# Kernel tuning notes

Measured on AMD Instinct MI355X. Metric: run time of the kernel, lower is better.

The kernel has to match this reference:

```python
import jax, jax.numpy as jnp
import numpy as np

B, S, D = 8, 2048, 2048
E, R, K = 8, 16, 2
NUM_TASKS, NUM_MODES = 4, 2
ALPHA = 16.0


def setup_inputs() -> dict:
    key = jax.random.key(0)
    k1, k2, k3, k4 = jax.random.split(key, 4)
    hidden_states = jax.random.normal(k1, (B, S, D), dtype=jnp.float32)
    gate_w = jax.random.normal(k2, (E, D), dtype=jnp.float32) * 0.01  # nn.init.normal_(std=0.01)
    # Soft-prior biases: fill(-1.0), strong prior 3.0 / 2.0 at configured (task, expert) / (mode, expert)
    tb = -np.ones((NUM_TASKS, E), dtype=np.float32)
    mb = -np.ones((NUM_MODES, E), dtype=np.float32)
    for e in range(E):
        tb[e % NUM_TASKS, e] = 3.0
        mb[e % NUM_MODES, e] = 2.0
    # LoRA params; lora_B is zero-init in torch but we use small random values for a nontrivial baseline
    lora_A = jax.random.normal(k3, (E, R, D), dtype=jnp.float32) * (1.0 / np.sqrt(D))
    lora_B = jax.random.normal(k4, (E, D, R), dtype=jnp.float32) * 0.02
    return {
        "hidden_states": hidden_states,
        "gate_w": gate_w,
        "task_bias": jnp.asarray(tb),
        "mode_bias": jnp.asarray(mb),
        "lora_A": lora_A,
        "lora_B": lora_B,
        "task_id": 1,
        "mode_id": 1,
    }


def reference(hidden_states, gate_w, task_bias, mode_bias, lora_A, lora_B, task_id, mode_id):
    scaling = ALPHA / R
    # Router: score = dynamic_gate(mean_pool(x)) + task_bias[t] + mode_bias[m]
    x_pooled = hidden_states.mean(axis=1)                       # [B, D]
    logits = x_pooled @ gate_w.T + task_bias[task_id] + mode_bias[mode_id]  # [B, E]
    top_v, top_i = jax.lax.top_k(logits, K)                     # [B, K]
    weights = jax.nn.softmax(top_v, axis=-1)                    # [B, K]
    # per-sample, per-expert combine weight: sum of top-k weights routed to that expert
    one_hot = jax.nn.one_hot(top_i, E, dtype=weights.dtype)     # [B, K, E]
    sw = jnp.einsum('bke,bk->be', one_hot, weights)             # [B, E]
    # LoRA experts: (x @ A_e^T) @ B_e^T * scaling, weighted-summed per sample
    mid = jnp.einsum('bsd,erd->besr', hidden_states, lora_A)    # [B, E, S, R] (small: R=16)
    out = jnp.einsum('be,besr,edr->bsd', sw, mid, lora_B) * scaling  # [B, S, D]
    return out
```

## Files before the change

kernel.cpp:

```cpp
#include <hip/hip_runtime.h>
#include <stdint.h>

typedef __attribute__((ext_vector_type(8))) short bf16x8;
typedef __attribute__((ext_vector_type(4))) float f32x4;
typedef __attribute__((ext_vector_type(16))) float f32x16;
typedef unsigned short ushort_t;

#define B_ 8
#define S_ 2048
#define D_ 2048
#define E_ 8
#define J_ 128
#define M_ 64
#define AROWS 136
#define ATILE (AROWS * 64)

static __device__ __forceinline__ unsigned short f2bf(float f) {
  union { float f; uint32_t u; } v; v.f = f;
  uint32_t u = v.u;
  return (unsigned short)((u + 0x7FFFu + ((u >> 16) & 1u)) >> 16);
}
static __device__ __forceinline__ float bf2f(ushort_t h) {
  union { uint32_t u; float f; } v; v.u = ((uint32_t)h) << 16;
  return v.f;
}
static __device__ __forceinline__ uint32_t pkbf(float a, float b) {
  uint32_t r;
  asm("v_cvt_pk_bf16_f32 %0, %1, %2" : "=v"(r) : "v"(a), "v"(b));
  return r;
}
static __device__ __forceinline__ int xswz(int row) {
  return (row & 7) ^ (((row >> 3) & 3) << 1);
}

#define GLL16(gsrc, ldst)                                                        \
  __builtin_amdgcn_global_load_lds(                                              \
      (const __attribute__((address_space(1))) void*)(gsrc),                     \
      (__attribute__((address_space(3))) void*)(ldst), 16, 0, 0)

#define SBAR() __builtin_amdgcn_sched_barrier(0)
#define VMWAIT(N)                                                                \
  do {                                                                           \
    asm volatile("s_waitcnt vmcnt(" #N ")" ::: "memory");                        \
    __builtin_amdgcn_sched_barrier(0);                                           \
  } while (0)
#define VMBAR(N)                                                                 \
  do {                                                                           \
    asm volatile("s_waitcnt vmcnt(" #N ") lgkmcnt(0)\n\ts_barrier" ::: "memory");\
    __builtin_amdgcn_sched_barrier(0);                                           \
  } while (0)

__global__ void k_prep(const float* __restrict__ lA, const float* __restrict__ lB,
                       const float* __restrict__ gw,
                       ushort_t* __restrict__ AgE, ushort_t* __restrict__ Bg) {
  int gid = blockIdx.x * blockDim.x + threadIdx.x;
  int stride = gridDim.x * blockDim.x;
  for (int o = gid; o < 32 * AROWS * 8; o += stride) {
    int kt = o / (AROWS * 8);
    int rem = o - kt * (AROWS * 8);
    int row = rem >> 3, c = rem & 7;
    int d = kt * 64 + (((c ^ xswz(row)) & 7) << 3);
    const float* src = (row < 128) ? (lA + (size_t)row * D_ + d)
                                   : (gw + (size_t)(row - 128) * D_ + d);
    float4 v0 = *(const float4*)src;
    float4 v1 = *(const float4*)(src + 4);
    bf16x8 outv;
    outv[0] = (short)f2bf(v0.x); outv[1] = (short)f2bf(v0.y);
    outv[2] = (short)f2bf(v0.z); outv[3] = (short)f2bf(v0.w);
    outv[4] = (short)f2bf(v1.x); outv[5] = (short)f2bf(v1.y);
    outv[6] = (short)f2bf(v1.z); outv[7] = (short)f2bf(v1.w);
    *(bf16x8*)&AgE[(size_t)o * 8] = outv;
  }
  for (int o4 = gid; o4 < (D_ * J_) / 4; o4 += stride) {
    int j4 = o4 & 31, dd = o4 >> 5;
    int e = j4 >> 2, r0 = (j4 & 3) * 4;
    float4 v = *(const float4*)(lB + ((size_t)e * D_ + dd) * 16 + r0);
    uint2 pk;
    pk.x = (uint32_t)f2bf(v.x) | ((uint32_t)f2bf(v.y) << 16);
    pk.y = (uint32_t)f2bf(v.z) | ((uint32_t)f2bf(v.w) << 16);
    ((uint2*)Bg)[o4] = pk;
  }
}

__global__ __launch_bounds__(512, 2) void k_mid(const float* __restrict__ x,
    const ushort_t* __restrict__ AgE, ushort_t* __restrict__ midb,
    float* __restrict__ lpart) {
  __shared__ ushort_t Ab[3][ATILE];
  __shared__ ushort_t Xb[2][4096];
  __shared__ float lsc[4][8];
  const int tid = threadIdx.x;
  const int w = tid >> 6, lane = tid & 63;
  const int l31 = lane & 31, hi = lane >> 5;
  const int jp = w & 1, xk = w >> 1;
  const int b = blockIdx.y, s0 = blockIdx.x * M_;
  const int xr = tid >> 3;
  const float* xsrc = x + ((size_t)(b * S_ + s0 + xr)) * D_ + (tid & 7) * 8;
  const int xwoff = xr * 64 + ((((tid & 7) ^ xswz(xr)) & 7) << 3);
  const int Xs = xswz(l31);

  f32x16 acc00 = {}, acc01 = {}, acc10 = {}, acc11 = {}, acc2 = {};

  auto stageA = [&](int buf, int kt) {
    const ushort_t* base = AgE + (size_t)kt * ATILE;
    GLL16(base + (size_t)tid * 8, &Ab[buf][tid * 8]);
    GLL16(base + (size_t)(512 + tid) * 8, &Ab[buf][(512 + tid) * 8]);
    GLL16(base + (size_t)(1024 + lane) * 8, &Ab[buf][(1024 + lane) * 8]);
  };
  auto loadX = [&](float4* r4, int t) {
    const float* p = xsrc + t * 64;
    r4[0] = *(const float4*)(p);
    r4[1] = *(const float4*)(p + 4);
  };
  auto cvtWrite = [&](int buf, const float4* r4) {
    uint4 q;
    q.x = pkbf(r4[0].x, r4[0].y); q.y = pkbf(r4[0].z, r4[0].w);
    q.z = pkbf(r4[1].x, r4[1].y); q.w = pkbf(r4[1].z, r4[1].w);
    *(uint4*)&Xb[buf][xwoff] = q;
  };
  auto computeTile = [&](int t, int ab) {
    const int cc = xk * 2 + hi;
    const int chs = (((cc ^ Xs) & 7) << 3);
    const ushort_t* Xp = &Xb[t & 1][l31 * 64 + chs];
    bf16x8 xf0 = *(const bf16x8*)Xp;
    bf16x8 xf1 = *(const bf16x8*)(Xp + 2048);
    const ushort_t* Ap = &Ab[ab][(jp * 64 + l31) * 64 + chs];
    bf16x8 af0 = *(const bf16x8*)Ap;
    bf16x8 af1 = *(const bf16x8*)(Ap + 2048);
    acc00 = __builtin_amdgcn_mfma_f32_32x32x16_bf16(af0, xf0, acc00, 0, 0, 0);
    acc10 = __builtin_amdgcn_mfma_f32_32x32x16_bf16(af0, xf1, acc10, 0, 0, 0);
    acc01 = __builtin_amdgcn_mfma_f32_32x32x16_bf16(af1, xf0, acc01, 0, 0, 0);
    acc11 = __builtin_amdgcn_mfma_f32_32x32x16_bf16(af1, xf1, acc11, 0, 0, 0);
    if (jp == 0) {
      bf16x8 af2 = *(const bf16x8*)&Ab[ab][(128 + l31) * 64 + chs];
      acc2 = __builtin_amdgcn_mfma_f32_32x32x16_bf16(af2, xf0, acc2, 0, 0, 0);
      acc2 = __builtin_amdgcn_mfma_f32_32x32x16_bf16(af2, xf1, acc2, 0, 0, 0);
    }
  };

  float4 xS0[2], xS1[2];
  loadX(xS0, 0); SBAR();
  stageA(0, 0);  SBAR();
  loadX(xS1, 1); SBAR();
  stageA(1, 1);  SBAR();
  VMWAIT(8);
  cvtWrite(0, xS0);
  VMBAR(5);

#define BODY(T, AB, ABN, XCUR, XNXT)                                             \
  do {                                                                           \
    loadX(XNXT, (T) + 2); SBAR();                                                \
    stageA((ABN), (T) + 2); SBAR();                                              \
    computeTile((T), (AB));                                                      \
    VMWAIT(8);                                                                   \
    cvtWrite(((T) + 1) & 1, XCUR);                                               \
    VMBAR(5);                                                                    \
  } while (0)

#pragma unroll 1
  for (int k6 = 0; k6 < 5; ++k6) {
    const int t0 = 6 * k6;
    BODY(t0 + 0, 0, 2, xS1, xS0);
    BODY(t0 + 1, 1, 0, xS0, xS1);
    BODY(t0 + 2, 2, 1, xS1, xS0);
    BODY(t0 + 3, 0, 2, xS0, xS1);
    BODY(t0 + 4, 1, 0, xS1, xS0);
    BODY(t0 + 5, 2, 1, xS0, xS1);
  }
#undef BODY
  computeTile(30, 0);
  VMWAIT(3);
  cvtWrite(1, xS1);
  VMBAR(0);
  computeTile(31, 1);

  __syncthreads();

  if (jp == 0) {
#pragma unroll
    for (int q = 0; q < 4; ++q) {
      float v = acc2[q];
      v += __shfl_xor(v, 1); v += __shfl_xor(v, 2); v += __shfl_xor(v, 4);
      v += __shfl_xor(v, 8); v += __shfl_xor(v, 16);
      if (l31 == 0) lsc[xk][hi * 4 + q] = v;
    }
  }

  float* const reg0 = (float*)&Ab[0][0];
  float* const reg1 = (float*)&Ab[1][0];
#pragma unroll 1
  for (int r = 1; r <= 3; ++r) {
    __syncthreads();
    if (xk == r) {
      float* p = jp ? reg1 : reg0;
#pragma unroll
      for (int i = 0; i < 16; ++i) {
        p[i * 64 + lane]        = acc00[i];
        p[(16 + i) * 64 + lane] = acc01[i];
        p[(32 + i) * 64 + lane] = acc10[i];
        p[(48 + i) * 64 + lane] = acc11[i];
      }
    }
    __syncthreads();
    if (xk == 0) {
      const float* p = jp ? reg1 : reg0;
#pragma unroll
      for (int i = 0; i < 16; ++i) {
        acc00[i] += p[i * 64 + lane];
        acc01[i] += p[(16 + i) * 64 + lane];
        acc10[i] += p[(32 + i) * 64 + lane];
        acc11[i] += p[(48 + i) * 64 + lane];
      }
    }
  }
  __syncthreads();

  if (xk == 0) {
#pragma unroll
    for (int sp = 0; sp < 2; ++sp) {
      ushort_t* mp = midb + ((size_t)(b * S_ + s0 + sp * 32 + l31)) * J_ + jp * 64 + 4 * hi;
#pragma unroll
      for (int G = 0; G < 4; ++G) {
        uint2 pA, pB;
        if (sp == 0) {
          pA.x = pkbf(acc00[G * 4 + 0], acc00[G * 4 + 1]);
          pA.y = pkbf(acc00[G * 4 + 2], acc00[G * 4 + 3]);
          pB.x = pkbf(acc01[G * 4 + 0], acc01[G * 4 + 1]);
          pB.y = pkbf(acc01[G * 4 + 2], acc01[G * 4 + 3]);
        } else {
          pA.x = pkbf(acc10[G * 4 + 0], acc10[G * 4 + 1]);
          pA.y = pkbf(acc10[G * 4 + 2], acc10[G * 4 + 3]);
          pB.x = pkbf(acc11[G * 4 + 0], acc11[G * 4 + 1]);
          pB.y = pkbf(acc11[G * 4 + 2], acc11[G * 4 + 3]);
        }
        *(uint2*)&mp[G * 8] = pA;
        *(uint2*)&mp[32 + G * 8] = pB;
      }
    }
  }
  if (w == 0 && lane < 8) {
    float s = lsc[0][lane] + lsc[1][lane] + lsc[2][lane] + lsc[3][lane];
    lpart[((size_t)(b * 32 + blockIdx.x)) * 8 + lane] = s;
  }
}

__global__ void k_router(const float* __restrict__ lpart,
                         const float* __restrict__ tb, const float* __restrict__ mb,
                         const int* __restrict__ task_p, const int* __restrict__ mode_p,
                         float* __restrict__ rinfo) {
  __shared__ float lg[64];
  const int t = threadIdx.x;
  const int b = t >> 3, e = t & 7;
  float s = 0.f;
  for (int k = 0; k < 32; ++k) s += lpart[((size_t)(b * 32 + k)) * 8 + e];
  lg[t] = s * (1.f / (float)S_) + tb[task_p[0] * E_ + e] + mb[mode_p[0] * E_ + e];
  __syncthreads();
  if (t < B_) {
    float v[8];
#pragma unroll
    for (int e2 = 0; e2 < 8; ++e2) v[e2] = lg[t * 8 + e2];
    int i1 = 0;
#pragma unroll
    for (int e2 = 1; e2 < 8; ++e2) if (v[e2] > v[i1]) i1 = e2;
    int i2 = (i1 == 0) ? 1 : 0;
#pragma unroll
    for (int e2 = 0; e2 < 8; ++e2) if (e2 != i1 && v[e2] > v[i2]) i2 = e2;
    float ex = __expf(v[i2] - v[i1]);
    float w1 = 1.f / (1.f + ex), w2 = ex * w1;
    float4 r;
    r.x = (float)i1; r.y = (float)i2; r.z = w1; r.w = w2;
    ((float4*)rinfo)[t] = r;
  }
}

__global__ __launch_bounds__(256) void k_comb(const ushort_t* __restrict__ midb,
    const float* __restrict__ rinfo, const ushort_t* __restrict__ Bg,
    float* __restrict__ out) {
  __shared__ ushort_t Bt[128][40];
  const int n = blockIdx.x, m = blockIdx.y, b = blockIdx.z;
  const int tid = threadIdx.x, w = tid >> 6, lane = tid & 63;
  const int lm = lane & 15, g = lane >> 4;

  const float4 ri = ((const float4*)rinfo)[b];
  const int i1 = (int)ri.x, i2 = (int)ri.y;
  const float w1 = ri.z, w2 = ri.w;

#pragma unroll
  for (int c = 0; c < 2; ++c) {
    int ci = c * 256 + tid;
    int d = ci >> 2, sub = ci & 3;
    int e = (sub & 2) ? i2 : i1;
    float sc = (sub & 2) ? w2 : w1;
    bf16x8 bv = *(const bf16x8*)(Bg + ((size_t)(n * 128 + d)) * J_ + e * 16 + (sub & 1) * 8);
    bf16x8 bw;
#pragma unroll
    for (int i = 0; i < 8; ++i) bw[i] = (short)f2bf(bf2f((ushort_t)bv[i]) * sc);
    *(bf16x8*)&Bt[d][sub * 8] = bw;
  }

  const int srow = m * 64 + w * 16 + lm;
  const int jw = (g < 2) ? (i1 * 16 + g * 8) : (i2 * 16 + (g - 2) * 8);
  bf16x8 pf = *(const bf16x8*)&midb[((size_t)(b * S_ + srow)) * J_ + jw];
  __syncthreads();

  f32x4 acc[8] = {};
#pragma unroll
  for (int nn = 0; nn < 8; ++nn) {
    bf16x8 af = *(const bf16x8*)&Bt[nn * 16 + lm][g * 8];
    acc[nn] = __builtin_amdgcn_mfma_f32_16x16x32_bf16(af, pf, acc[nn], 0, 0, 0);
  }

  float* op = out + ((size_t)(b * S_ + srow)) * D_ + n * 128;
#pragma unroll
  for (int nn = 0; nn < 8; ++nn)
    *(f32x4*)&op[nn * 16 + g * 4] = acc[nn];
}

extern "C" void kernel_launch(void* const* d_in, const int* in_sizes, int n_in,
                              void* d_out, int out_size, void* d_ws, size_t ws_size,
                              hipStream_t stream) {
  const float* x    = (const float*)d_in[0];
  const float* gw   = (const float*)d_in[1];
  const float* tb   = (const float*)d_in[2];
  const float* mb   = (const float*)d_in[3];
  const float* lA   = (const float*)d_in[4];
  const float* lB   = (const float*)d_in[5];
  const int* task_p = (const int*)d_in[6];
  const int* mode_p = (const int*)d_in[7];
  float* out = (float*)d_out;
  char* ws = (char*)d_ws;
  ushort_t* midb = (ushort_t*)ws;
  ushort_t* AgE  = (ushort_t*)(ws + 4194304);
  ushort_t* Bg   = (ushort_t*)(ws + 4751360);
  float* lpart   = (float*)(ws + 5275648);
  float* rinfo   = (float*)(ws + 5283840);

  hipLaunchKernelGGL(k_prep, dim3(256), dim3(256), 0, stream, lA, lB, gw, AgE, Bg);
  hipLaunchKernelGGL(k_mid, dim3(32, 8), dim3(512), 0, stream, x, AgE, midb, lpart);
  hipLaunchKernelGGL(k_router, dim3(1), dim3(64), 0, stream,
                     lpart, tb, mb, task_p, mode_p, rinfo);
  hipLaunchKernelGGL(k_comb, dim3(16, 32, 8), dim3(256), 0, stream, midb, rinfo, Bg, out);
}
```

Measured before the change: 76.57 us.

## Split k_mid reduction over D across two blocks and sum halves in combine

k_mid now launches a third grid dimension that splits the D reduction into two halves, doubling the block count from 256 to 512 so more CUs get work. Each block writes a partial bf16 mid buffer, and k_comb sums the two halves before its MFMA. Warps are remapped so each owns one 32-row slice and a K-subset, which cuts the in-block cross-warp reduction from three rounds to one. Launch bounds are raised to 4 blocks per CU. The cost is twice the mid write/read traffic, an extra bf16 rounding of the partials, and higher register pressure.

Result: slower. 79.71 us (+4.1%).

```diff
diff --git a/kernel.cpp b/kernel.cpp
--- a/kernel.cpp
+++ b/kernel.cpp
@@ -14,6 +14,7 @@
 #define M_ 64
 #define AROWS 136
 #define ATILE (AROWS * 64)
+#define MIDSZ ((size_t)B_ * S_ * J_)
 
 static __device__ __forceinline__ unsigned short f2bf(float f) {
   union { float f; uint32_t u; } v; v.f = f;
@@ -82,7 +83,7 @@
   }
 }
 
-__global__ __launch_bounds__(512, 2) void k_mid(const float* __restrict__ x,
+__global__ __launch_bounds__(512, 4) void k_mid(const float* __restrict__ x,
     const ushort_t* __restrict__ AgE, ushort_t* __restrict__ midb,
     float* __restrict__ lpart) {
   __shared__ ushort_t Ab[3][ATILE];
@@ -91,17 +92,19 @@
   const int tid = threadIdx.x;
   const int w = tid >> 6, lane = tid & 63;
   const int l31 = lane & 31, hi = lane >> 5;
-  const int jp = w & 1, xk = w >> 1;
+  const int jp = w & 1, sp = (w >> 1) & 1, kk = w >> 2;
   const int b = blockIdx.y, s0 = blockIdx.x * M_;
+  const int kh = blockIdx.z;
   const int xr = tid >> 3;
-  const float* xsrc = x + ((size_t)(b * S_ + s0 + xr)) * D_ + (tid & 7) * 8;
+  const float* xsrc = x + ((size_t)(b * S_ + s0 + xr)) * D_ + kh * 1024 + (tid & 7) * 8;
   const int xwoff = xr * 64 + ((((tid & 7) ^ xswz(xr)) & 7) << 3);
   const int Xs = xswz(l31);
-
-  f32x16 acc00 = {}, acc01 = {}, acc10 = {}, acc11 = {}, acc2 = {};
-
-  auto stageA = [&](int buf, int kt) {
-    const ushort_t* base = AgE + (size_t)kt * ATILE;
+  const ushort_t* Abase = AgE + (size_t)kh * 16 * ATILE;
+
+  f32x16 acc00 = {}, acc01 = {}, acc2 = {};
+
+  auto stageA = [&](int buf, int t) {
+    const ushort_t* base = Abase + (size_t)t * ATILE;
     GLL16(base + (size_t)tid * 8, &Ab[buf][tid * 8]);
     GLL16(base + (size_t)(512 + tid) * 8, &Ab[buf][(512 + tid) * 8]);
     GLL16(base + (size_t)(1024 + lane) * 8, &Ab[buf][(1024 + lane) * 8]);
@@ -118,22 +121,22 @@
     *(uint4*)&Xb[buf][xwoff] = q;
   };
   auto computeTile = [&](int t, int ab) {
-    const int cc = xk * 2 + hi;
-    const int chs = (((cc ^ Xs) & 7) << 3);
-    const ushort_t* Xp = &Xb[t & 1][l31 * 64 + chs];
-    bf16x8 xf0 = *(const bf16x8*)Xp;
-    bf16x8 xf1 = *(const bf16x8*)(Xp + 2048);
-    const ushort_t* Ap = &Ab[ab][(jp * 64 + l31) * 64 + chs];
-    bf16x8 af0 = *(const bf16x8*)Ap;
-    bf16x8 af1 = *(const bf16x8*)(Ap + 2048);
-    acc00 = __builtin_amdgcn_mfma_f32_32x32x16_bf16(af0, xf0, acc00, 0, 0, 0);
-    acc10 = __builtin_amdgcn_mfma_f32_32x32x16_bf16(af0, xf1, acc10, 0, 0, 0);
-    acc01 = __builtin_amdgcn_mfma_f32_32x32x16_bf16(af1, xf0, acc01, 0, 0, 0);
-    acc11 = __builtin_amdgcn_mfma_f32_32x32x16_bf16(af1, xf1, acc11, 0, 0, 0);
-    if (jp == 0) {
-      bf16x8 af2 = *(const bf16x8*)&Ab[ab][(128 + l31) * 64 + chs];
-      acc2 = __builtin_amdgcn_mfma_f32_32x32x16_bf16(af2, xf0, acc2, 0, 0, 0);
-      acc2 = __builtin_amdgcn_mfma_f32_32x32x16_bf16(af2, xf1, acc2, 0, 0, 0);
+    const int xbuf = t & 1;
+#pragma unroll
+    for (int k2 = 0; k2 < 2; ++k2) {
+      const int ks = kk * 2 + k2;
+      const int cc = ks * 2 + hi;
+      const int chs = (((cc ^ Xs) & 7) << 3);
+      bf16x8 xf = *(const bf16x8*)&Xb[xbuf][(sp * 32 + l31) * 64 + chs];
+      const ushort_t* Ap = &Ab[ab][(jp * 64 + l31) * 64 + chs];
+      bf16x8 af0 = *(const bf16x8*)Ap;
+      bf16x8 af1 = *(const bf16x8*)(Ap + 2048);
+      acc00 = __builtin_amdgcn_mfma_f32_32x32x16_bf16(af0, xf, acc00, 0, 0, 0);
+      acc01 = __builtin_amdgcn_mfma_f32_32x32x16_bf16(af1, xf, acc01, 0, 0, 0);
+      if (jp == 0) {
+        bf16x8 af2 = *(const bf16x8*)&Ab[ab][(128 + l31) * 64 + chs];
+        acc2 = __builtin_amdgcn_mfma_f32_32x32x16_bf16(af2, xf, acc2, 0, 0, 0);
+      }
     }
   };
 
@@ -156,22 +159,24 @@
     VMBAR(5);                                                                    \
   } while (0)
 
+  BODY(0, 0, 2, xS1, xS0);
 #pragma unroll 1
-  for (int k6 = 0; k6 < 5; ++k6) {
+  for (int k6 = 0; k6 < 2; ++k6) {
     const int t0 = 6 * k6;
-    BODY(t0 + 0, 0, 2, xS1, xS0);
     BODY(t0 + 1, 1, 0, xS0, xS1);
     BODY(t0 + 2, 2, 1, xS1, xS0);
     BODY(t0 + 3, 0, 2, xS0, xS1);
     BODY(t0 + 4, 1, 0, xS1, xS0);
     BODY(t0 + 5, 2, 1, xS0, xS1);
-  }
+    BODY(t0 + 6, 0, 2, xS1, xS0);
+  }
+  BODY(13, 1, 0, xS0, xS1);
 #undef BODY
-  computeTile(30, 0);
+  computeTile(14, 2);
   VMWAIT(3);
   cvtWrite(1, xS1);
   VMBAR(0);
-  computeTile(31, 1);
+  computeTile(15, 0);
 
   __syncthreads();
 
@@ -181,65 +186,42 @@
       float v = acc2[q];
       v += __shfl_xor(v, 1); v += __shfl_xor(v, 2); v += __shfl_xor(v, 4);
       v += __shfl_xor(v, 8); v += __shfl_xor(v, 16);
-      if (l31 == 0) lsc[xk][hi * 4 + q] = v;
-    }
-  }
-
-  float* const reg0 = (float*)&Ab[0][0];
-  float* const reg1 = (float*)&Ab[1][0];
-#pragma unroll 1
-  for (int r = 1; r <= 3; ++r) {
-    __syncthreads();
-    if (xk == r) {
-      float* p = jp ? reg1 : reg0;
-#pragma unroll
-      for (int i = 0; i < 16; ++i) {
-        p[i * 64 + lane]        = acc00[i];
-        p[(16 + i) * 64 + lane] = acc01[i];
-        p[(32 + i) * 64 + lane] = acc10[i];
-        p[(48 + i) * 64 + lane] = acc11[i];
-      }
-    }
-    __syncthreads();
-    if (xk == 0) {
-      const float* p = jp ? reg1 : reg0;
-#pragma unroll
-      for (int i = 0; i < 16; ++i) {
-        acc00[i] += p[i * 64 + lane];
-        acc01[i] += p[(16 + i) * 64 + lane];
-        acc10[i] += p[(32 + i) * 64 + lane];
-        acc11[i] += p[(48 + i) * 64 + lane];
-      }
+      if (l31 == 0) lsc[sp + 2 * kk][hi * 4 + q] = v;
+    }
+  }
+  float* const scr = (float*)&Ab[0][0];
+  if (kk == 1) {
+    float* p = scr + ((size_t)(w & 3)) * 2048;
+#pragma unroll
+    for (int i = 0; i < 16; ++i) {
+      p[i * 64 + lane]        = acc00[i];
+      p[(16 + i) * 64 + lane] = acc01[i];
     }
   }
   __syncthreads();
-
-  if (xk == 0) {
-#pragma unroll
-    for (int sp = 0; sp < 2; ++sp) {
-      ushort_t* mp = midb + ((size_t)(b * S_ + s0 + sp * 32 + l31)) * J_ + jp * 64 + 4 * hi;
-#pragma unroll
-      for (int G = 0; G < 4; ++G) {
-        uint2 pA, pB;
-        if (sp == 0) {
-          pA.x = pkbf(acc00[G * 4 + 0], acc00[G * 4 + 1]);
-          pA.y = pkbf(acc00[G * 4 + 2], acc00[G * 4 + 3]);
-          pB.x = pkbf(acc01[G * 4 + 0], acc01[G * 4 + 1]);
-          pB.y = pkbf(acc01[G * 4 + 2], acc01[G * 4 + 3]);
-        } else {
-          pA.x = pkbf(acc10[G * 4 + 0], acc10[G * 4 + 1]);
-          pA.y = pkbf(acc10[G * 4 + 2], acc10[G * 4 + 3]);
-          pB.x = pkbf(acc11[G * 4 + 0], acc11[G * 4 + 1]);
-          pB.y = pkbf(acc11[G * 4 + 2], acc11[G * 4 + 3]);
-        }
-        *(uint2*)&mp[G * 8] = pA;
-        *(uint2*)&mp[32 + G * 8] = pB;
-      }
+  if (kk == 0) {
+    const float* p = scr + ((size_t)(w & 3)) * 2048;
+#pragma unroll
+    for (int i = 0; i < 16; ++i) {
+      acc00[i] += p[i * 64 + lane];
+      acc01[i] += p[(16 + i) * 64 + lane];
+    }
+    ushort_t* mp = midb + (size_t)kh * MIDSZ +
+                   ((size_t)(b * S_ + s0 + sp * 32 + l31)) * J_ + jp * 64 + 4 * hi;
+#pragma unroll
+    for (int G = 0; G < 4; ++G) {
+      uint2 pA, pB;
+      pA.x = pkbf(acc00[G * 4 + 0], acc00[G * 4 + 1]);
+      pA.y = pkbf(acc00[G * 4 + 2], acc00[G * 4 + 3]);
+      pB.x = pkbf(acc01[G * 4 + 0], acc01[G * 4 + 1]);
+      pB.y = pkbf(acc01[G * 4 + 2], acc01[G * 4 + 3]);
+      *(uint2*)&mp[G * 8] = pA;
+      *(uint2*)&mp[32 + G * 8] = pB;
     }
   }
   if (w == 0 && lane < 8) {
     float s = lsc[0][lane] + lsc[1][lane] + lsc[2][lane] + lsc[3][lane];
-    lpart[((size_t)(b * 32 + blockIdx.x)) * 8 + lane] = s;
+    lpart[((size_t)(b * 64 + blockIdx.x * 2 + kh)) * 8 + lane] = s;
   }
 }
 
@@ -251,7 +233,7 @@
   const int t = threadIdx.x;
   const int b = t >> 3, e = t & 7;
   float s = 0.f;
-  for (int k = 0; k < 32; ++k) s += lpart[((size_t)(b * 32 + k)) * 8 + e];
+  for (int k = 0; k < 64; ++k) s += lpart[((size_t)(b * 64 + k)) * 8 + e];
   lg[t] = s * (1.f / (float)S_) + tb[task_p[0] * E_ + e] + mb[mode_p[0] * E_ + e];
   __syncthreads();
   if (t < B_) {
@@ -299,7 +281,13 @@
 
   const int srow = m * 64 + w * 16 + lm;
   const int jw = (g < 2) ? (i1 * 16 + g * 8) : (i2 * 16 + (g - 2) * 8);
-  bf16x8 pf = *(const bf16x8*)&midb[((size_t)(b * S_ + srow)) * J_ + jw];
+  const ushort_t* mp0 = midb + ((size_t)(b * S_ + srow)) * J_ + jw;
+  bf16x8 p0 = *(const bf16x8*)mp0;
+  bf16x8 p1 = *(const bf16x8*)(mp0 + MIDSZ);
+  bf16x8 pf;
+#pragma unroll
+  for (int i = 0; i < 8; ++i)
+    pf[i] = (short)f2bf(bf2f((ushort_t)p0[i]) + bf2f((ushort_t)p1[i]));
   __syncthreads();
 
   f32x4 acc[8] = {};
@@ -329,13 +317,13 @@
   float* out = (float*)d_out;
   char* ws = (char*)d_ws;
   ushort_t* midb = (ushort_t*)ws;
-  ushort_t* AgE  = (ushort_t*)(ws + 4194304);
-  ushort_t* Bg   = (ushort_t*)(ws + 4751360);
-  float* lpart   = (float*)(ws + 5275648);
-  float* rinfo   = (float*)(ws + 5283840);
+  ushort_t* AgE  = (ushort_t*)(ws + 8388608);
+  ushort_t* Bg   = (ushort_t*)(ws + 8945664);
+  float* lpart   = (float*)(ws + 9469952);
+  float* rinfo   = (float*)(ws + 9486336);
 
   hipLaunchKernelGGL(k_prep, dim3(256), dim3(256), 0, stream, lA, lB, gw, AgE, Bg);
-  hipLaunchKernelGGL(k_mid, dim3(32, 8), dim3(512), 0, stream, x, AgE, midb, lpart);
+  hipLaunchKernelGGL(k_mid, dim3(32, 8, 2), dim3(512), 0, stream, x, AgE, midb, lpart);
   hipLaunchKernelGGL(k_router, dim3(1), dim3(64), 0, stream,
                      lpart, tb, mb, task_p, mode_p, rinfo);
   hipLaunchKernelGGL(k_comb, dim3(16, 32, 8), dim3(256), 0, stream, midb, rinfo, Bg, out);
```
